# Optimization experiments

Hardware: AMD Instinct MI355X
Metric: run time of the kernel (lower is better)

Reference implementation:

```python
import jax, jax.numpy as jnp
import numpy as np

SHIFT = 1  # module draws +/-1 at init; fixed to +1 for determinism


def setup_inputs() -> dict:
    key = jax.random.key(0)
    k1, k2 = jax.random.split(key)
    x = jax.random.normal(k1, (1, 64, 56, 56), dtype=jnp.float32)
    w = jax.random.normal(k2, (64, 32, 2, 3), dtype=jnp.float32)
    return {"x": x, "w": w}


def reference(x, w):
    # einsum 'iklj -> ilkj': (1,64,56,56) -> (1,56,64,56)
    t = jnp.transpose(x, (0, 2, 1, 3))
    # split channels 64 -> (2,32)
    t = t.reshape(1, 56, 2, 32, 56)
    # fuse (56,2) -> 112 and circular-shift by +1 along it
    t = t.reshape(1, 112, 32, 56)
    t = jnp.roll(t, SHIFT, axis=1)
    t = t.reshape(1, 56, 2, 32, 56)
    # circular shift along the last spatial axis
    t = jnp.roll(t, SHIFT, axis=4)
    # unfold with kernel (3,1), padding (1,0) over the last axis (length 56):
    # zero-pad then take 3 sliding windows -> new axis k of size 3
    p = jnp.pad(t, ((0, 0), (0, 0), (0, 0), (0, 0), (1, 1)))
    t_unf = jnp.stack([p[..., 0:56], p[..., 1:57], p[..., 2:58]], axis=4)  # (1,56,2,32,3,56)
    # contraction over j=2, l=32, k=3 -> output (1,56,64,56)
    y = jnp.einsum('mnjlko,iljk->mino', t_unf, w)
    return y
```

## Files before the change

### kernel.cpp

```cpp
#include <hip/hip_runtime.h>


#define PAD 68

__global__ __launch_bounds__(128) void shiftconv_kernel(
    const float* __restrict__ x, const float* __restrict__ w, float* __restrict__ out)
{
    const int n   = blockIdx.x >> 2;
    const int ig  = blockIdx.x & 3;
    const int tid = threadIdx.x;

    __shared__ float Az[58 * PAD];
    __shared__ float Ws[16 * 3 * PAD];

    const int hprev = (n + 55) % 56;

    if (tid < PAD) {
        Az[tid] = 0.f;
        Az[57 * PAD + tid] = 0.f;
    }

    for (int idx = tid; idx < 64 * 14; idx += 128) {
        const int c = idx / 14, q = idx % 14;
        const int h = (c < 32) ? n : hprev;
        const float4 v = *(const float4*)(x + c * 3136 + h * 56 + 4 * q);
        const float vv[4] = {v.x, v.y, v.z, v.w};
        #pragma unroll
        for (int j = 0; j < 4; ++j) {
            const int s = 4 * q + j;
            const int e = 1 + ((s + 1) % 56);
            Az[e * PAD + c] = vv[j];
        }
    }

    for (int idx = tid; idx < 16 * 192; idx += 128) {
        const int ii = idx / 192, r = idx % 192;
        const int k = r / 64, c = r % 64;
        const int i = ig * 16 + ii;
        const int l = (c < 32) ? c : c - 32;
        const int j = (c < 32) ? 1 : 0;
        Ws[(ii * 3 + k) * PAD + c] = w[i * 192 + l * 6 + j * 3 + k];
    }
    __syncthreads();

    const int ii = tid >> 3;
    const int og = tid & 7;
    const int ob = og * 7;

    float acc[7] = {0.f, 0.f, 0.f, 0.f, 0.f, 0.f, 0.f};
    const float* Wi = &Ws[ii * 3 * PAD];
    const float* Ab = &Az[ob * PAD];

    #pragma unroll 4
    for (int c4 = 0; c4 < 64; c4 += 4) {
        float4 wv[3], av[9];
        #pragma unroll
        for (int k = 0; k < 3; ++k) wv[k] = *(const float4*)(Wi + k * PAD + c4);
        #pragma unroll
        for (int d = 0; d < 9; ++d) av[d] = *(const float4*)(Ab + d * PAD + c4);
        #pragma unroll
        for (int oo = 0; oo < 7; ++oo) {
            #pragma unroll
            for (int k = 0; k < 3; ++k) {
                acc[oo] += wv[k].x * av[oo + k].x + wv[k].y * av[oo + k].y
                         + wv[k].z * av[oo + k].z + wv[k].w * av[oo + k].w;
            }
        }
    }

    float* op = out + (ig * 16 + ii) * 3136 + n * 56 + ob;
    #pragma unroll
    for (int oo = 0; oo < 7; ++oo) op[oo] = acc[oo];
}

extern "C" void kernel_launch(void* const* d_in, const int* in_sizes, int n_in,
                              void* d_out, int out_size, void* d_ws, size_t ws_size,
                              hipStream_t stream) {
    const float* x = (const float*)d_in[0];
    const float* w = (const float*)d_in[1];
    float* out = (float*)d_out;

    shiftconv_kernel<<<224, 128, 0, stream>>>(x, w, out);
}
```

Baseline: 14.13 us.

## Split channel reduction across thread halves and compute two output channels per thread

Each thread now computes two output channels over half of the 64 input channels, so every loaded activation float4 feeds two weight sets. The two channel halves are combined through a small shared-memory buffer after an extra barrier, and the channel loop is fully unrolled over 8 steps. This cuts shared-memory activation loads per FMA. The cost is more registers, an extra sync, and a reduction step in which only half the threads write output.

```diff
diff --git a/kernel.cpp b/kernel.cpp
--- a/kernel.cpp
+++ b/kernel.cpp
@@ -12,6 +12,7 @@
 
     __shared__ float Az[58 * PAD];
     __shared__ float Ws[16 * 3 * PAD];
+    __shared__ float Rr[64 * 17];
 
     const int hprev = (n + 55) % 56;
 
@@ -43,34 +44,56 @@
     }
     __syncthreads();
 
-    const int ii = tid >> 3;
+    const int ch = tid >> 6;
+    const int p  = (tid >> 3) & 7;
     const int og = tid & 7;
     const int ob = og * 7;
 
-    float acc[7] = {0.f, 0.f, 0.f, 0.f, 0.f, 0.f, 0.f};
-    const float* Wi = &Ws[ii * 3 * PAD];
-    const float* Ab = &Az[ob * PAD];
+    float acc[2][7] = {};
+    const float* W0 = &Ws[(2 * p) * 3 * PAD + ch * 32];
+    const float* W1 = &Ws[(2 * p + 1) * 3 * PAD + ch * 32];
+    const float* Ab = &Az[ob * PAD + ch * 32];
 
-    #pragma unroll 4
-    for (int c4 = 0; c4 < 64; c4 += 4) {
-        float4 wv[3], av[9];
+    #pragma unroll
+    for (int j = 0; j < 8; ++j) {
+        const int c4 = 4 * j;
+        float4 wv0[3], wv1[3], av[9];
         #pragma unroll
-        for (int k = 0; k < 3; ++k) wv[k] = *(const float4*)(Wi + k * PAD + c4);
+        for (int k = 0; k < 3; ++k) {
+            wv0[k] = *(const float4*)(W0 + k * PAD + c4);
+            wv1[k] = *(const float4*)(W1 + k * PAD + c4);
+        }
         #pragma unroll
         for (int d = 0; d < 9; ++d) av[d] = *(const float4*)(Ab + d * PAD + c4);
         #pragma unroll
         for (int oo = 0; oo < 7; ++oo) {
             #pragma unroll
             for (int k = 0; k < 3; ++k) {
-                acc[oo] += wv[k].x * av[oo + k].x + wv[k].y * av[oo + k].y
-                         + wv[k].z * av[oo + k].z + wv[k].w * av[oo + k].w;
+                const float4 a = av[oo + k];
+                acc[0][oo] += wv0[k].x * a.x + wv0[k].y * a.y + wv0[k].z * a.z + wv0[k].w * a.w;
+                acc[1][oo] += wv1[k].x * a.x + wv1[k].y * a.y + wv1[k].z * a.z + wv1[k].w * a.w;
             }
         }
     }
 
-    float* op = out + (ig * 16 + ii) * 3136 + n * 56 + ob;
-    #pragma unroll
-    for (int oo = 0; oo < 7; ++oo) op[oo] = acc[oo];
+    const int r = tid & 63;
+    if (ch == 1) {
+        #pragma unroll
+        for (int i2 = 0; i2 < 2; ++i2)
+            #pragma unroll
+            for (int oo = 0; oo < 7; ++oo)
+                Rr[r * 17 + i2 * 8 + oo] = acc[i2][oo];
+    }
+    __syncthreads();
+    if (ch == 0) {
+        #pragma unroll
+        for (int i2 = 0; i2 < 2; ++i2) {
+            float* op = out + (ig * 16 + 2 * p + i2) * 3136 + n * 56 + ob;
+            #pragma unroll
+            for (int oo = 0; oo < 7; ++oo)
+                op[oo] = acc[i2][oo] + Rr[r * 17 + i2 * 8 + oo];
+        }
+    }
 }
 
 extern "C" void kernel_launch(void* const* d_in, const int* in_sizes, int n_in,
```

Result: faster. 12.74 us (-9.8%).
